# Optimization experiments

Hardware: AMD Instinct MI355X
Metric: run time of the kernel (lower is better)

Reference implementation:

```python
import jax, jax.numpy as jnp
import numpy as np

U = I = 4096; E = 128; K = 4; D = E // K; R = 3; B = 512; L = 100
LAMB = 0.5; L2NORM = 1e-4; EPS = 1e-8


def _l2norm(x, axis):
    n = jnp.sqrt(jnp.sum(x * x, axis=axis, keepdims=True))
    return x / jnp.maximum(n, 1e-12)


def setup_inputs() -> dict:
    key = jax.random.key(0)
    ks = jax.random.split(key, 16)
    def adj(k, shape, p=0.01):
        return jax.random.bernoulli(k, p, shape).astype(jnp.float32)
    relation_mats = adj(ks[0], (R, U, I))
    item_graphs = adj(ks[1], (R, I, I))
    train_matrix = relation_mats[0]
    inp = {
        "user": jax.random.randint(ks[2], (B, 1), 0, U),
        "item": jax.random.randint(ks[3], (B, L), 0, I),
        "user_embedding": jax.random.normal(ks[4], (U, E), jnp.float32) * 0.1,
        "item_embedding": jax.random.normal(ks[5], (I, E), jnp.float32) * 0.1,
        "mgnn_weight": jax.random.normal(ks[6], (R,), jnp.float32),
        "item_behaviour_W": jax.random.normal(ks[7], (R, E, E), jnp.float32) * 0.05,
        "item_propagate_W": jax.random.normal(ks[8], (R, E, E), jnp.float32) * 0.05,
        "W": jax.random.normal(ks[9], (E, E), jnp.float32) * 0.05,
        "W_K": jax.random.normal(ks[10], (K, D, E), jnp.float32) * 0.05,
        "B_K": jax.random.normal(ks[11], (K, D), jnp.float32) * 0.05,
        "train_matrix": train_matrix,
        "relation_mats": relation_mats,
        "item_graphs": item_graphs,
        "item_graph_degree": item_graphs.sum(axis=2, keepdims=True),  # [R,I,1]
        "user_behaviour_degree": relation_mats.sum(axis=2).T,  # [U,R]
    }
    return inp


def reference(user, item, user_embedding, item_embedding, mgnn_weight,
              item_behaviour_W, item_propagate_W, W, W_K, B_K,
              train_matrix, relation_mats, item_graphs, item_graph_degree,
              user_behaviour_degree):
    # behaviour weighting: [U,R]
    total_weight = user_behaviour_degree @ mgnn_weight[:, None]  # [U,1]
    ubw = user_behaviour_degree * mgnn_weight[None, :] / (total_weight + EPS)

    # K-head projections (relation-independent; original recomputes identically per relation)
    s_i = _l2norm(jax.nn.relu(jnp.einsum('kde,ie->kdi', W_K, item_embedding) + B_K[..., None]), axis=1)  # [K,D,I]
    s_u0 = _l2norm(jax.nn.relu(jnp.einsum('kde,ue->kdu', W_K, user_embedding) + B_K[..., None]), axis=1)  # [K,D,U]
    s_u0 = jnp.transpose(s_u0, (2, 0, 1))  # [U,K,D]

    ue_blocks = user_embedding.reshape(U, K, D)
    logits = jnp.einsum('ukd,kdi->kui', ue_blocks, s_i)  # [K,U,I]
    r = jax.nn.softmax(logits, axis=0)  # exp / sum over K heads

    user_feature = jnp.zeros((U, E), user_embedding.dtype)
    score2 = jnp.zeros((B, L), user_embedding.dtype)
    for i in range(R):
        rel = relation_mats[i]  # [U,I]
        # item-item propagation
        tip = ((item_graphs[i] @ item_embedding) / (item_graph_degree[i] + EPS)) @ item_propagate_W[i]  # [I,E]
        tmp_item_emb = tip[item]  # [B,L,E]
        # attention-weighted user-item propagation per head
        s_u = s_u0 + jnp.einsum('kui,kdi->ukd', r * rel[None], s_i)  # [U,K,D]
        tun = _l2norm(s_u, axis=2).reshape(U, E)  # tmp_user_neighbour
        tuinp = (rel @ tip) / (user_behaviour_degree[:, i:i + 1] + EPS)  # [U,E]
        user_feature = user_feature + ubw[:, i:i + 1] * tun
        proj = tuinp @ item_behaviour_W[i]  # [U,E]
        score2 = score2 + jnp.sum(proj[user[:, 0]][:, None, :] * tmp_item_emb, axis=2)
    score2 = score2 / R

    item_feature = (train_matrix.T @ user_embedding) @ W  # [I,E]
    user_feature = user_feature @ W  # [U,E]

    uf = user_feature[user[:, 0]][:, None, :]  # [B,1,E]
    itf = item_feature[item]  # [B,L,E]
    score1 = jnp.sum(uf * itf, axis=2)  # [B,L]
    scores = score1 + LAMB * score2
    L2_loss = L2NORM * (L * jnp.sum(uf ** 2) + jnp.sum(itf ** 2))
    return scores, L2_loss
```

## Files before the change

### kernel.cpp

```cpp
#include <hip/hip_runtime.h>

#define NU 4096
#define NI 4096
#define NR 3
#define NB 512
#define NL 100
#define FEPS 1e-8f

#define WS_SI    0
#define WS_AGG   524288
#define WS_TIP   2097152
#define WS_UEW   3670016
#define WS_ITEMF 4194304
#define WS_WTUN  4718592
#define WS_PROJ  4915200
#define WS_UF    5111808
#define WS_UF2P  5177344
#define WS_ITF2P 5177856
#define WS_BMT   5190656

__global__ void k_si(const float* __restrict__ iemb, const float* __restrict__ WK,
                     const float* __restrict__ BK, float* __restrict__ si) {
  int i = blockIdx.x;
  __shared__ __align__(16) float embs[128];
  int t = threadIdx.x;
  if (t < 32) ((float4*)embs)[t] = ((const float4*)(iemb + (size_t)i * 128))[t];
  __syncthreads();
  float acc = BK[t];
  const float4* wk4 = (const float4*)(WK + (size_t)t * 128);
  const float4* e4 = (const float4*)embs;
#pragma unroll 8
  for (int c = 0; c < 32; ++c) {
    float4 w = wk4[c], v = e4[c];
    acc += w.x * v.x + w.y * v.y + w.z * v.z + w.w * v.w;
  }
  acc = fmaxf(acc, 0.f);
  float sq = acc * acc;
#pragma unroll
  for (int m = 1; m <= 16; m <<= 1) sq += __shfl_xor(sq, m);
  si[(size_t)i * 128 + t] = acc / fmaxf(sqrtf(sq), 1e-12f);
}

__global__ void k_agg(const float* __restrict__ G, const float* __restrict__ emb,
                      const float* __restrict__ deg, float* __restrict__ agg) {
  int bid = blockIdx.x;
  const float4* row4 = (const float4*)(G + (size_t)bid * NI);
  __shared__ int nz[512];
  __shared__ int cnt;
  __shared__ float4 red[8][32];
  int t = threadIdx.x;
  if (t == 0) cnt = 0;
  __syncthreads();
#pragma unroll
  for (int c = 0; c < 4; ++c) {
    int idx4 = c * 256 + t;
    float4 v = row4[idx4];
    int j0 = idx4 << 2;
    if (v.x != 0.f) nz[atomicAdd(&cnt, 1)] = j0;
    if (v.y != 0.f) nz[atomicAdd(&cnt, 1)] = j0 + 1;
    if (v.z != 0.f) nz[atomicAdd(&cnt, 1)] = j0 + 2;
    if (v.w != 0.f) nz[atomicAdd(&cnt, 1)] = j0 + 3;
  }
  __syncthreads();
  int n = min(cnt, 512);
  int g = t >> 5, f = t & 31;
  float4 acc = {0.f, 0.f, 0.f, 0.f};
  const float4* emb4 = (const float4*)emb;
  for (int p = g; p < n; p += 8) {
    float4 v = emb4[(size_t)nz[p] * 32 + f];
    acc.x += v.x; acc.y += v.y; acc.z += v.z; acc.w += v.w;
  }
  red[g][f] = acc;
  __syncthreads();
  if (t < 32) {
    float4 s = red[0][t];
#pragma unroll
    for (int q = 1; q < 8; ++q) {
      float4 v = red[q][t];
      s.x += v.x; s.y += v.y; s.z += v.z; s.w += v.w;
    }
    float inv = 1.f / (deg[bid] + FEPS);
    s.x *= inv; s.y *= inv; s.z *= inv; s.w *= inv;
    ((float4*)(agg + (size_t)bid * 128))[t] = s;
  }
}

__global__ void k_bmm(const float* __restrict__ agg, const float* __restrict__ ipW,
                      const float* __restrict__ uemb, const float* __restrict__ Wm,
                      float* __restrict__ tip, float* __restrict__ uew) {
  int batch = blockIdx.x >> 8, rb = blockIdx.x & 255;
  const float* in;
  const float* Wp;
  float* out;
  if (batch < 3) {
    in = agg + (size_t)batch * NI * 128;
    Wp = ipW + (size_t)batch * 16384;
    out = tip + (size_t)batch * NI * 128;
  } else {
    in = uemb; Wp = Wm; out = uew;
  }
  __shared__ __align__(16) float inl[16][128];
  int t = threadIdx.x;
  const float4* in4 = (const float4*)(in + (size_t)rb * 2048);
  for (int c = t; c < 512; c += 256) ((float4*)inl)[c] = in4[c];
  __syncthreads();
  int c = t & 127, g = t >> 7;
  float acc[8];
#pragma unroll
  for (int rr = 0; rr < 8; ++rr) acc[rr] = 0.f;
  for (int e = 0; e < 128; ++e) {
    float wv = Wp[e * 128 + c];
#pragma unroll
    for (int rr = 0; rr < 8; ++rr) acc[rr] += inl[g * 8 + rr][e] * wv;
  }
#pragma unroll
  for (int rr = 0; rr < 8; ++rr) out[((size_t)rb * 16 + g * 8 + rr) * 128 + c] = acc[rr];
}

__global__ void k_bits(const float* __restrict__ tm, unsigned long long* __restrict__ bmT) {
  int row = blockIdx.x;
  int t = threadIdx.x;
  __shared__ unsigned short sh[256];
  const float4* r4 = (const float4*)(tm + (size_t)row * NI);
  unsigned int m = 0;
#pragma unroll
  for (int q = 0; q < 4; ++q) {
    float4 v = r4[t * 4 + q];
    int b = q * 4;
    if (v.x != 0.f) m |= (1u << b);
    if (v.y != 0.f) m |= (1u << (b + 1));
    if (v.z != 0.f) m |= (1u << (b + 2));
    if (v.w != 0.f) m |= (1u << (b + 3));
  }
  sh[t] = (unsigned short)m;
  __syncthreads();
  if (t < 64) {
    unsigned long long mm = (unsigned long long)sh[4 * t]
      | ((unsigned long long)sh[4 * t + 1] << 16)
      | ((unsigned long long)sh[4 * t + 2] << 32)
      | ((unsigned long long)sh[4 * t + 3] << 48);
    bmT[(size_t)t * NU + row] = mm;
  }
}

__global__ void k_itemf_csc(const unsigned long long* __restrict__ bmT,
                            const float* __restrict__ uew, float* __restrict__ itemf) {
  int i = blockIdx.x;
  int ct = i >> 6;
  unsigned long long bitm = 1ull << (i & 63);
  __shared__ int lst[192];
  __shared__ int cnt;
  __shared__ float red[3][128];
  int t = threadIdx.x;
  if (t == 0) cnt = 0;
  __syncthreads();
  const unsigned long long* col = bmT + (size_t)ct * NU;
#pragma unroll
  for (int cc = 0; cc < 16; ++cc) {
    unsigned long long m = col[cc * 256 + t];
    if (m & bitm) lst[atomicAdd(&cnt, 1)] = cc * 256 + t;
  }
  __syncthreads();
  int n = min(cnt, 192);
  int w = t >> 6, l = t & 63;
  float ax = 0.f, ay = 0.f;
  const float2* uew2 = (const float2*)uew;
  for (int p = w; p < n; p += 4) {
    float2 v = uew2[(size_t)lst[p] * 64 + l];
    ax += v.x; ay += v.y;
  }
  if (w > 0) { red[w - 1][2 * l] = ax; red[w - 1][2 * l + 1] = ay; }
  __syncthreads();
  if (w == 0) {
    float2 o;
    o.x = ax + red[0][2 * l] + red[1][2 * l] + red[2][2 * l];
    o.y = ay + red[0][2 * l + 1] + red[1][2 * l + 1] + red[2][2 * l + 1];
    ((float2*)(itemf + (size_t)i * 128))[l] = o;
  }
}

__global__ void k_user(const int* __restrict__ user, const float* __restrict__ relm,
                       const float* __restrict__ si, const float* __restrict__ tip,
                       const float* __restrict__ uemb, const float* __restrict__ WK,
                       const float* __restrict__ BK, const float* __restrict__ ibW,
                       const float* __restrict__ ubd, const float* __restrict__ mw,
                       float* __restrict__ wtun, float* __restrict__ proj) {
  int bid = blockIdx.x;
  int r = bid >> 9, b = bid & 511;
  int u = user[b];
  const float* rel = relm + ((size_t)r * NU + u) * NI;
  __shared__ int nz[512];
  __shared__ int cnt;
  __shared__ __align__(16) float uel[128];
  __shared__ float redA[4][128];
  __shared__ float redB[4][128];
  __shared__ float tu[128];
  int t = threadIdx.x;
  if (t == 0) cnt = 0;
  if (t < 32) ((float4*)uel)[t] = ((const float4*)(uemb + (size_t)u * 128))[t];
  __syncthreads();
  const float4* rel4 = (const float4*)rel;
#pragma unroll
  for (int c = 0; c < 4; ++c) {
    int idx4 = c * 256 + t;
    float4 v = rel4[idx4];
    int j0 = idx4 << 2;
    if (v.x != 0.f) nz[atomicAdd(&cnt, 1)] = j0;
    if (v.y != 0.f) nz[atomicAdd(&cnt, 1)] = j0 + 1;
    if (v.z != 0.f) nz[atomicAdd(&cnt, 1)] = j0 + 2;
    if (v.w != 0.f) nz[atomicAdd(&cnt, 1)] = j0 + 3;
  }
  __syncthreads();
  int n = min(cnt, 512);
  int wid = t >> 6, lane = t & 63;
  int k = lane >> 4;
  float2 myue = ((const float2*)uel)[lane];
  float sux = 0.f, suy = 0.f, tpx = 0.f, tpy = 0.f;
  const float2* si2 = (const float2*)si;
  const float2* tip2 = (const float2*)(tip + (size_t)r * NI * 128);
  for (int p = wid; p < n; p += 4) {
    int i = nz[p];
    float2 sv = si2[(size_t)i * 64 + lane];
    float lg = myue.x * sv.x + myue.y * sv.y;
    lg += __shfl_xor(lg, 1);
    lg += __shfl_xor(lg, 2);
    lg += __shfl_xor(lg, 4);
    lg += __shfl_xor(lg, 8);
    float l0 = __shfl(lg, 0), l1 = __shfl(lg, 16), l2 = __shfl(lg, 32), l3 = __shfl(lg, 48);
    float mx = fmaxf(fmaxf(l0, l1), fmaxf(l2, l3));
    float e0 = __expf(l0 - mx), e1 = __expf(l1 - mx), e2 = __expf(l2 - mx), e3 = __expf(l3 - mx);
    float inv = 1.f / (e0 + e1 + e2 + e3);
    float myr = (k == 0 ? e0 : k == 1 ? e1 : k == 2 ? e2 : e3) * inv;
    sux += myr * sv.x;
    suy += myr * sv.y;
    float2 tv = tip2[(size_t)i * 64 + lane];
    tpx += tv.x;
    tpy += tv.y;
  }
  redA[wid][2 * lane] = sux; redA[wid][2 * lane + 1] = suy;
  redB[wid][2 * lane] = tpx; redB[wid][2 * lane + 1] = tpy;
  __syncthreads();
  if (t < 128) {
    float suv = redA[0][t] + redA[1][t] + redA[2][t] + redA[3][t];
    float tipv = redB[0][t] + redB[1][t] + redB[2][t] + redB[3][t];
    float a = BK[t];
    const float4* wk4 = (const float4*)(WK + (size_t)t * 128);
    const float4* ue4 = (const float4*)uel;
#pragma unroll 8
    for (int c = 0; c < 32; ++c) {
      float4 w = wk4[c], v = ue4[c];
      a += w.x * v.x + w.y * v.y + w.z * v.z + w.w * v.w;
    }
    a = fmaxf(a, 0.f);
    float sq = a * a;
#pragma unroll
    for (int m = 1; m <= 16; m <<= 1) sq += __shfl_xor(sq, m);
    float su = a / fmaxf(sqrtf(sq), 1e-12f) + suv;
    float sq2 = su * su;
#pragma unroll
    for (int m = 1; m <= 16; m <<= 1) sq2 += __shfl_xor(sq2, m);
    float tun = su / fmaxf(sqrtf(sq2), 1e-12f);
    float d0 = ubd[u * 3], d1 = ubd[u * 3 + 1], d2 = ubd[u * 3 + 2];
    float w0 = mw[0], w1 = mw[1], w2 = mw[2];
    float tw = d0 * w0 + d1 * w1 + d2 * w2;
    float dr = (r == 0 ? d0 : r == 1 ? d1 : d2);
    float wr = (r == 0 ? w0 : r == 1 ? w1 : w2);
    wtun[(size_t)(b * 3 + r) * 128 + t] = (dr * wr / (tw + FEPS)) * tun;
    tu[t] = tipv / (dr + FEPS);
  }
  __syncthreads();
  int ep = t & 127, hh = t >> 7;
  const float* Wb = ibW + (size_t)r * 16384;
  float pacc = 0.f;
  for (int e = hh * 64; e < hh * 64 + 64; ++e) pacc += tu[e] * Wb[e * 128 + ep];
  redA[hh][ep] = pacc;
  __syncthreads();
  if (hh == 0) proj[(size_t)(b * 3 + r) * 128 + ep] = redA[0][ep] + redA[1][ep];
}

__global__ void k_uf(const float* __restrict__ wtun, const float* __restrict__ Wm,
                     float* __restrict__ uf, float* __restrict__ uf2p) {
  int b = blockIdx.x, t = threadIdx.x;
  __shared__ float comb[128];
  __shared__ float part[2];
  comb[t] = wtun[(size_t)(b * 3) * 128 + t] + wtun[(size_t)(b * 3 + 1) * 128 + t] +
            wtun[(size_t)(b * 3 + 2) * 128 + t];
  __syncthreads();
  float acc = 0.f;
  for (int e = 0; e < 128; ++e) acc += comb[e] * Wm[e * 128 + t];
  uf[(size_t)b * 128 + t] = acc;
  float sq = acc * acc;
#pragma unroll
  for (int m = 1; m <= 32; m <<= 1) sq += __shfl_xor(sq, m);
  if ((t & 63) == 0) part[t >> 6] = sq;
  __syncthreads();
  if (t == 0) uf2p[b] = part[0] + part[1];
}

__global__ void k_score(const int* __restrict__ item, const float* __restrict__ itemf,
                        const float* __restrict__ uf, const float* __restrict__ tip,
                        const float* __restrict__ proj, float* __restrict__ out,
                        float* __restrict__ itf2p) {
  int t = threadIdx.x, wid = t >> 6, lane = t & 63;
  int idx = blockIdx.x * 4 + wid;
  int b = idx / NL;
  int it = item[idx];
  float2 av = ((const float2*)(itemf + (size_t)it * 128))[lane];
  float2 cv = ((const float2*)(uf + (size_t)b * 128))[lane];
  float s1 = av.x * cv.x + av.y * cv.y;
  float sqi = av.x * av.x + av.y * av.y;
  float s2 = 0.f;
#pragma unroll
  for (int r = 0; r < 3; ++r) {
    float2 tv = ((const float2*)(tip + ((size_t)r * NI + it) * 128))[lane];
    float2 pv = ((const float2*)(proj + (size_t)(b * 3 + r) * 128))[lane];
    s2 += tv.x * pv.x + tv.y * pv.y;
  }
#pragma unroll
  for (int m = 1; m <= 32; m <<= 1) {
    s1 += __shfl_xor(s1, m);
    s2 += __shfl_xor(s2, m);
    sqi += __shfl_xor(sqi, m);
  }
  if (lane == 0) out[idx] = s1 + 0.5f * (s2 * (1.f / 3.f));
  __shared__ float sh[4];
  if (lane == 0) sh[wid] = sqi;
  __syncthreads();
  if (t == 0) itf2p[blockIdx.x] = sh[0] + sh[1] + sh[2] + sh[3];
}

__global__ void k_final(const float* __restrict__ itf2p, const float* __restrict__ uf2p,
                        float* __restrict__ out) {
  int t = threadIdx.x;
  float v = 0.f;
  for (int i = t; i < 12800; i += 256) v += itf2p[i];
  float vu = 0.f;
  for (int i = t; i < NB; i += 256) vu += uf2p[i];
  v += 100.f * vu;
#pragma unroll
  for (int m = 1; m <= 32; m <<= 1) v += __shfl_xor(v, m);
  __shared__ float sh[4];
  if ((t & 63) == 0) sh[t >> 6] = v;
  __syncthreads();
  if (t == 0) out[NB * NL] = 1e-4f * (sh[0] + sh[1] + sh[2] + sh[3]);
}

extern "C" void kernel_launch(void* const* d_in, const int* in_sizes, int n_in,
                              void* d_out, int out_size, void* d_ws, size_t ws_size,
                              hipStream_t stream) {
  (void)in_sizes; (void)n_in; (void)out_size; (void)ws_size;
  const int* user = (const int*)d_in[0];
  const int* item = (const int*)d_in[1];
  const float* uemb = (const float*)d_in[2];
  const float* iemb = (const float*)d_in[3];
  const float* mw = (const float*)d_in[4];
  const float* ibW = (const float*)d_in[5];
  const float* ipW = (const float*)d_in[6];
  const float* Wm = (const float*)d_in[7];
  const float* WK = (const float*)d_in[8];
  const float* BK = (const float*)d_in[9];
  const float* tm = (const float*)d_in[10];
  const float* relm = (const float*)d_in[11];
  const float* ig = (const float*)d_in[12];
  const float* igd = (const float*)d_in[13];
  const float* ubd = (const float*)d_in[14];
  float* out = (float*)d_out;
  float* ws = (float*)d_ws;
  unsigned long long* bmT = (unsigned long long*)(ws + WS_BMT);

  k_si<<<NI, 128, 0, stream>>>(iemb, WK, BK, ws + WS_SI);
  k_bits<<<NU, 256, 0, stream>>>(tm, bmT);
  k_agg<<<NR * NI, 256, 0, stream>>>(ig, iemb, igd, ws + WS_AGG);
  k_bmm<<<1024, 256, 0, stream>>>(ws + WS_AGG, ipW, uemb, Wm, ws + WS_TIP, ws + WS_UEW);
  k_itemf_csc<<<NI, 256, 0, stream>>>(bmT, ws + WS_UEW, ws + WS_ITEMF);
  k_user<<<NR * NB, 256, 0, stream>>>(user, relm, ws + WS_SI, ws + WS_TIP, uemb, WK, BK,
                                      ibW, ubd, mw, ws + WS_WTUN, ws + WS_PROJ);
  k_uf<<<NB, 128, 0, stream>>>(ws + WS_WTUN, Wm, ws + WS_UF, ws + WS_UF2P);
  k_score<<<12800, 256, 0, stream>>>(item, ws + WS_ITEMF, ws + WS_UF, ws + WS_TIP,
                                     ws + WS_PROJ, out, ws + WS_ITF2P);
  k_final<<<1, 256, 0, stream>>>(ws + WS_ITF2P, ws + WS_UF2P, out);
}
```

Measured before the change: 199.0 us.

## Reassociate item propagation matmul before gather and merge four launches into two

Applies the projection W_ip to item embeddings before the sparse neighbour aggregation, so tip = (G @ (emb @ W)) / deg instead of ((G @ emb)/deg) @ W. This lets the dense matmul and the s_i projection share one launch, and the bitmask build and sparse aggregation share a second launch. The intermediate agg buffer and two kernel launches go away, at the cost of slightly different floating-point summation order. The bitmask kernel now reads coalesced float4s per lane and packs nibbles.

```diff
diff --git a/kernel.cpp b/kernel.cpp
--- a/kernel.cpp
+++ b/kernel.cpp
@@ -8,7 +8,7 @@
 #define FEPS 1e-8f
 
 #define WS_SI    0
-#define WS_AGG   524288
+#define WS_EMBW  524288
 #define WS_TIP   2097152
 #define WS_UEW   3670016
 #define WS_ITEMF 4194304
@@ -19,127 +19,131 @@
 #define WS_ITF2P 5177856
 #define WS_BMT   5190656
 
-__global__ void k_si(const float* __restrict__ iemb, const float* __restrict__ WK,
-                     const float* __restrict__ BK, float* __restrict__ si) {
-  int i = blockIdx.x;
-  __shared__ __align__(16) float embs[128];
-  int t = threadIdx.x;
-  if (t < 32) ((float4*)embs)[t] = ((const float4*)(iemb + (size_t)i * 128))[t];
-  __syncthreads();
-  float acc = BK[t];
-  const float4* wk4 = (const float4*)(WK + (size_t)t * 128);
-  const float4* e4 = (const float4*)embs;
+__global__ void k_bmm_si(const float* __restrict__ iemb, const float* __restrict__ ipW,
+                         const float* __restrict__ uemb, const float* __restrict__ Wm,
+                         const float* __restrict__ WK, const float* __restrict__ BK,
+                         float* __restrict__ embW, float* __restrict__ uew,
+                         float* __restrict__ si) {
+  __shared__ __align__(16) float shbuf[2048];
+  int t = threadIdx.x;
+  int bid = blockIdx.x;
+  if (bid < 1024) {
+    int batch = bid >> 8, rb = bid & 255;
+    const float* in;
+    const float* Wp;
+    float* out;
+    if (batch < 3) {
+      in = iemb;
+      Wp = ipW + (size_t)batch * 16384;
+      out = embW + (size_t)batch * NI * 128;
+    } else {
+      in = uemb; Wp = Wm; out = uew;
+    }
+    const float4* in4 = (const float4*)(in + (size_t)rb * 2048);
+    for (int c = t; c < 512; c += 256) ((float4*)shbuf)[c] = in4[c];
+    __syncthreads();
+    int c = t & 127, g = t >> 7;
+    float acc[8];
+#pragma unroll
+    for (int rr = 0; rr < 8; ++rr) acc[rr] = 0.f;
+    for (int e = 0; e < 128; ++e) {
+      float wv = Wp[e * 128 + c];
+#pragma unroll
+      for (int rr = 0; rr < 8; ++rr) acc[rr] += shbuf[(g * 8 + rr) * 128 + e] * wv;
+    }
+#pragma unroll
+    for (int rr = 0; rr < 8; ++rr) out[((size_t)rb * 16 + g * 8 + rr) * 128 + c] = acc[rr];
+  } else {
+    int tl = t & 127, half = t >> 7;
+    int item = (bid - 1024) * 2 + half;
+    float* embs = shbuf + half * 128;
+    if (tl < 32) ((float4*)embs)[tl] = ((const float4*)(iemb + (size_t)item * 128))[tl];
+    __syncthreads();
+    float acc = BK[tl];
+    const float4* wk4 = (const float4*)(WK + (size_t)tl * 128);
+    const float4* e4 = (const float4*)embs;
 #pragma unroll 8
-  for (int c = 0; c < 32; ++c) {
-    float4 w = wk4[c], v = e4[c];
-    acc += w.x * v.x + w.y * v.y + w.z * v.z + w.w * v.w;
-  }
-  acc = fmaxf(acc, 0.f);
-  float sq = acc * acc;
-#pragma unroll
-  for (int m = 1; m <= 16; m <<= 1) sq += __shfl_xor(sq, m);
-  si[(size_t)i * 128 + t] = acc / fmaxf(sqrtf(sq), 1e-12f);
-}
-
-__global__ void k_agg(const float* __restrict__ G, const float* __restrict__ emb,
-                      const float* __restrict__ deg, float* __restrict__ agg) {
+    for (int c = 0; c < 32; ++c) {
+      float4 w = wk4[c], v = e4[c];
+      acc += w.x * v.x + w.y * v.y + w.z * v.z + w.w * v.w;
+    }
+    acc = fmaxf(acc, 0.f);
+    float sq = acc * acc;
+#pragma unroll
+    for (int m = 1; m <= 16; m <<= 1) sq += __shfl_xor(sq, m);
+    si[(size_t)item * 128 + tl] = acc / fmaxf(sqrtf(sq), 1e-12f);
+  }
+}
+
+__global__ void k_scan(const float* __restrict__ tm, const float* __restrict__ G,
+                       const float* __restrict__ deg, const float* __restrict__ embW,
+                       unsigned long long* __restrict__ bmT, float* __restrict__ tip) {
   int bid = blockIdx.x;
-  const float4* row4 = (const float4*)(G + (size_t)bid * NI);
-  __shared__ int nz[512];
-  __shared__ int cnt;
-  __shared__ float4 red[8][32];
-  int t = threadIdx.x;
-  if (t == 0) cnt = 0;
-  __syncthreads();
-#pragma unroll
-  for (int c = 0; c < 4; ++c) {
-    int idx4 = c * 256 + t;
-    float4 v = row4[idx4];
-    int j0 = idx4 << 2;
-    if (v.x != 0.f) nz[atomicAdd(&cnt, 1)] = j0;
-    if (v.y != 0.f) nz[atomicAdd(&cnt, 1)] = j0 + 1;
-    if (v.z != 0.f) nz[atomicAdd(&cnt, 1)] = j0 + 2;
-    if (v.w != 0.f) nz[atomicAdd(&cnt, 1)] = j0 + 3;
-  }
-  __syncthreads();
-  int n = min(cnt, 512);
-  int g = t >> 5, f = t & 31;
-  float4 acc = {0.f, 0.f, 0.f, 0.f};
-  const float4* emb4 = (const float4*)emb;
-  for (int p = g; p < n; p += 8) {
-    float4 v = emb4[(size_t)nz[p] * 32 + f];
-    acc.x += v.x; acc.y += v.y; acc.z += v.z; acc.w += v.w;
-  }
-  red[g][f] = acc;
-  __syncthreads();
-  if (t < 32) {
-    float4 s = red[0][t];
-#pragma unroll
-    for (int q = 1; q < 8; ++q) {
-      float4 v = red[q][t];
-      s.x += v.x; s.y += v.y; s.z += v.z; s.w += v.w;
-    }
-    float inv = 1.f / (deg[bid] + FEPS);
-    s.x *= inv; s.y *= inv; s.z *= inv; s.w *= inv;
-    ((float4*)(agg + (size_t)bid * 128))[t] = s;
-  }
-}
-
-__global__ void k_bmm(const float* __restrict__ agg, const float* __restrict__ ipW,
-                      const float* __restrict__ uemb, const float* __restrict__ Wm,
-                      float* __restrict__ tip, float* __restrict__ uew) {
-  int batch = blockIdx.x >> 8, rb = blockIdx.x & 255;
-  const float* in;
-  const float* Wp;
-  float* out;
-  if (batch < 3) {
-    in = agg + (size_t)batch * NI * 128;
-    Wp = ipW + (size_t)batch * 16384;
-    out = tip + (size_t)batch * NI * 128;
+  int t = threadIdx.x;
+  if (bid < NU) {
+    __shared__ unsigned char nib[4][256];
+    const float4* r4 = (const float4*)(tm + (size_t)bid * NI);
+#pragma unroll
+    for (int q = 0; q < 4; ++q) {
+      float4 v = r4[q * 256 + t];
+      unsigned m = 0;
+      if (v.x != 0.f) m |= 1u;
+      if (v.y != 0.f) m |= 2u;
+      if (v.z != 0.f) m |= 4u;
+      if (v.w != 0.f) m |= 8u;
+      nib[q][t] = (unsigned char)m;
+    }
+    __syncthreads();
+    if (t < 64) {
+      unsigned long long mm = 0;
+#pragma unroll
+      for (int j = 0; j < 16; ++j) {
+        int e = t * 16 + j;
+        mm |= (unsigned long long)nib[e >> 8][e & 255] << (4 * j);
+      }
+      bmT[(size_t)t * NU + bid] = mm;
+    }
   } else {
-    in = uemb; Wp = Wm; out = uew;
-  }
-  __shared__ __align__(16) float inl[16][128];
-  int t = threadIdx.x;
-  const float4* in4 = (const float4*)(in + (size_t)rb * 2048);
-  for (int c = t; c < 512; c += 256) ((float4*)inl)[c] = in4[c];
-  __syncthreads();
-  int c = t & 127, g = t >> 7;
-  float acc[8];
-#pragma unroll
-  for (int rr = 0; rr < 8; ++rr) acc[rr] = 0.f;
-  for (int e = 0; e < 128; ++e) {
-    float wv = Wp[e * 128 + c];
-#pragma unroll
-    for (int rr = 0; rr < 8; ++rr) acc[rr] += inl[g * 8 + rr][e] * wv;
-  }
-#pragma unroll
-  for (int rr = 0; rr < 8; ++rr) out[((size_t)rb * 16 + g * 8 + rr) * 128 + c] = acc[rr];
-}
-
-__global__ void k_bits(const float* __restrict__ tm, unsigned long long* __restrict__ bmT) {
-  int row = blockIdx.x;
-  int t = threadIdx.x;
-  __shared__ unsigned short sh[256];
-  const float4* r4 = (const float4*)(tm + (size_t)row * NI);
-  unsigned int m = 0;
-#pragma unroll
-  for (int q = 0; q < 4; ++q) {
-    float4 v = r4[t * 4 + q];
-    int b = q * 4;
-    if (v.x != 0.f) m |= (1u << b);
-    if (v.y != 0.f) m |= (1u << (b + 1));
-    if (v.z != 0.f) m |= (1u << (b + 2));
-    if (v.w != 0.f) m |= (1u << (b + 3));
-  }
-  sh[t] = (unsigned short)m;
-  __syncthreads();
-  if (t < 64) {
-    unsigned long long mm = (unsigned long long)sh[4 * t]
-      | ((unsigned long long)sh[4 * t + 1] << 16)
-      | ((unsigned long long)sh[4 * t + 2] << 32)
-      | ((unsigned long long)sh[4 * t + 3] << 48);
-    bmT[(size_t)t * NU + row] = mm;
+    int gid = bid - NU;
+    int r = gid >> 12;
+    const float4* row4 = (const float4*)(G + (size_t)gid * NI);
+    __shared__ int nz[512];
+    __shared__ int cnt;
+    __shared__ float4 red[8][32];
+    if (t == 0) cnt = 0;
+    __syncthreads();
+#pragma unroll
+    for (int c = 0; c < 4; ++c) {
+      int idx4 = c * 256 + t;
+      float4 v = row4[idx4];
+      int j0 = idx4 << 2;
+      if (v.x != 0.f) nz[atomicAdd(&cnt, 1)] = j0;
+      if (v.y != 0.f) nz[atomicAdd(&cnt, 1)] = j0 + 1;
+      if (v.z != 0.f) nz[atomicAdd(&cnt, 1)] = j0 + 2;
+      if (v.w != 0.f) nz[atomicAdd(&cnt, 1)] = j0 + 3;
+    }
+    __syncthreads();
+    int n = min(cnt, 512);
+    int g = t >> 5, f = t & 31;
+    float4 acc = {0.f, 0.f, 0.f, 0.f};
+    const float4* e4 = (const float4*)(embW + (size_t)r * NI * 128);
+    for (int p = g; p < n; p += 8) {
+      float4 v = e4[(size_t)nz[p] * 32 + f];
+      acc.x += v.x; acc.y += v.y; acc.z += v.z; acc.w += v.w;
+    }
+    red[g][f] = acc;
+    __syncthreads();
+    if (t < 32) {
+      float4 s = red[0][t];
+#pragma unroll
+      for (int q = 1; q < 8; ++q) {
+        float4 v = red[q][t];
+        s.x += v.x; s.y += v.y; s.z += v.z; s.w += v.w;
+      }
+      float inv = 1.f / (deg[gid] + FEPS);
+      s.x *= inv; s.y *= inv; s.z *= inv; s.w *= inv;
+      ((float4*)(tip + (size_t)gid * 128))[t] = s;
+    }
   }
 }
 
@@ -368,10 +372,9 @@
   float* ws = (float*)d_ws;
   unsigned long long* bmT = (unsigned long long*)(ws + WS_BMT);
 
-  k_si<<<NI, 128, 0, stream>>>(iemb, WK, BK, ws + WS_SI);
-  k_bits<<<NU, 256, 0, stream>>>(tm, bmT);
-  k_agg<<<NR * NI, 256, 0, stream>>>(ig, iemb, igd, ws + WS_AGG);
-  k_bmm<<<1024, 256, 0, stream>>>(ws + WS_AGG, ipW, uemb, Wm, ws + WS_TIP, ws + WS_UEW);
+  k_bmm_si<<<3072, 256, 0, stream>>>(iemb, ipW, uemb, Wm, WK, BK,
+                                     ws + WS_EMBW, ws + WS_UEW, ws + WS_SI);
+  k_scan<<<NU + NR * NI, 256, 0, stream>>>(tm, ig, igd, ws + WS_EMBW, bmT, ws + WS_TIP);
   k_itemf_csc<<<NI, 256, 0, stream>>>(bmT, ws + WS_UEW, ws + WS_ITEMF);
   k_user<<<NR * NB, 256, 0, stream>>>(user, relm, ws + WS_SI, ws + WS_TIP, uemb, WK, BK,
                                       ibW, ubd, mw, ws + WS_WTUN, ws + WS_PROJ);
```

Measured after the change: 186.6 us. 6.2% less time.
